# Kernel optimization log

Measured on AMD Instinct MI355X. Metric: run time of the kernel, lower is better.

The kernel has to match this reference:

```python
import jax, jax.numpy as jnp
import numpy as np
from jax import lax

B, C, H, W = 4, 256, 64, 64
O = 256
EPS = 1e-5


def setup_inputs() -> dict:
    key = jax.random.key(0)
    ks = jax.random.split(key, 20)
    s = 0.02
    d = {
        'input1': jax.random.normal(ks[0], (B, C, H, W), jnp.float32),
        'input2': jax.random.normal(ks[1], (B, C, H, W), jnp.float32),
        'wq1': jax.random.normal(ks[2], (C // 8, C), jnp.float32) * s,
        'bq1': jnp.zeros((C // 8,), jnp.float32),
        'wk1': jax.random.normal(ks[3], (C // 4, C), jnp.float32) * s,
        'bk1': jnp.zeros((C // 4,), jnp.float32),
        'wv1': jax.random.normal(ks[4], (C, C), jnp.float32) * s,
        'bv1': jnp.zeros((C,), jnp.float32),
        'wq2': jax.random.normal(ks[5], (C // 8, C), jnp.float32) * s,
        'bq2': jnp.zeros((C // 8,), jnp.float32),
        'wk2': jax.random.normal(ks[6], (C // 4, C), jnp.float32) * s,
        'bk2': jnp.zeros((C // 4,), jnp.float32),
        'wv2': jax.random.normal(ks[7], (C, C), jnp.float32) * s,
        'bv2': jnp.zeros((C,), jnp.float32),
        'gamma': jnp.asarray([0.1], jnp.float32),
        'w_cat': jax.random.normal(ks[8], (O, 2 * C, 3, 3), jnp.float32) * s,
        'bn_scale': jnp.ones((O,), jnp.float32),
        'bn_bias': jnp.zeros((O,), jnp.float32),
        'bn_mean': jnp.zeros((O,), jnp.float32),
        'bn_var': jnp.ones((O,), jnp.float32),
    }
    return d


def _conv1x1(x, w, b):
    # x: [B,C,H,W], w: [Co,C] -> [B,Co,H,W]
    return jnp.einsum('bchw,oc->bohw', x, w) + b[None, :, None, None]


def reference(input1, input2, wq1, bq1, wk1, bk1, wv1, bv1,
              wq2, bq2, wk2, bk2, wv2, bv2, gamma, w_cat,
              bn_scale, bn_bias, bn_mean, bn_var):
    b, c, h, w = input1.shape
    hw = h * w
    q1 = _conv1x1(input1, wq1, bq1)
    k1 = _conv1x1(input1, wk1, bk1).reshape(b, -1, hw)
    v1 = _conv1x1(input1, wv1, bv1).reshape(b, -1, hw)
    q2 = _conv1x1(input2, wq2, bq2)
    k2 = _conv1x1(input2, wk2, bk2).reshape(b, -1, hw)
    v2 = _conv1x1(input2, wv2, bv2).reshape(b, -1, hw)
    # concat q heads along channel -> [B, C/4, HW] -> [B, HW, C/4]
    q = jnp.concatenate([q1, q2], axis=1).reshape(b, -1, hw).transpose(0, 2, 1)
    # branch 1: [B,HW,HW] scores (no scaling, as in source)
    attn1 = jax.nn.softmax(jnp.einsum('bnc,bcm->bnm', q, k1), axis=-1)
    out1 = jnp.einsum('bcm,bnm->bcn', v1, attn1).reshape(b, c, h, w)
    out1 = gamma[0] * out1 + input1
    # branch 2
    attn2 = jax.nn.softmax(jnp.einsum('bnc,bcm->bnm', q, k2), axis=-1)
    out2 = jnp.einsum('bcm,bnm->bcn', v2, attn2).reshape(b, c, h, w)
    out2 = gamma[0] * out2 + input2
    # conv_cat: 3x3 conv (no bias) + BatchNorm (eval stats) + ReLU
    cat = jnp.concatenate([out1, out2], axis=1)
    conv = lax.conv_general_dilated(cat, w_cat, (1, 1), 'SAME',
                                    dimension_numbers=('NCHW', 'OIHW', 'NCHW'))
    inv = bn_scale / jnp.sqrt(bn_var + EPS)
    bn = conv * inv[None, :, None, None] + (bn_bias - bn_mean * inv)[None, :, None, None]
    feat_sum = jax.nn.relu(bn)
    return (feat_sum, out1, out2)
```

## Files before the change

kernel.cpp:

```cpp
#include <hip/hip_runtime.h>
#include <hip/hip_bf16.h>

#define HW 4096

#define KT_OFF   1048576
#define WTP_OFF  1572864
#define O1_OFF   4194304
#define WVB_OFF  1179648

typedef short v8s  __attribute__((ext_vector_type(8)));
typedef float v16f __attribute__((ext_vector_type(16)));

#define LSTR 72
#define ZSTR 264
#define CPAD 20
#define PL_ROWS 128
#define PL_SZ  (2 * PL_ROWS * LSTR)
#define XP_SZ  (2 * 256 * LSTR)

__device__ __forceinline__ unsigned short f2b(float f) {
    unsigned u = __float_as_uint(f);
    return (unsigned short)((u + 0x7fffu + ((u >> 16) & 1u)) >> 16);
}
__device__ __forceinline__ unsigned cvt_pk_bf16(float lo, float hi) {
    float2 f2; f2.x = lo; f2.y = hi;
    __hip_bfloat162 h = __float22bfloat162_rn(f2);
    unsigned r;
    __builtin_memcpy(&r, &h, 4);
    return r;
}
__device__ __forceinline__ v8s load8(const unsigned short* p) {
    union { uint2 u[2]; v8s v; } t;
    t.u[0] = *(const uint2*)p;
    t.u[1] = *(const uint2*)(p + 4);
    return t.v;
}

__global__ __launch_bounds__(256) void wprep_proj(
    const float* __restrict__ wq1, const float* __restrict__ wk1, const float* __restrict__ wv1,
    const float* __restrict__ wq2, const float* __restrict__ wk2, const float* __restrict__ wv2,
    float* __restrict__ wtp) {
    int idx = blockIdx.x * 256 + threadIdx.x;
    if (idx >= 2 * 256 * 352) return;
    int sel = idx / 90112;
    int r   = idx - sel * 90112;
    int c   = r / 352;
    int co  = r - c * 352;
    const float* w; int row;
    if (co < 32)      { w = sel ? wq2 : wq1; row = co; }
    else if (co < 96) { w = sel ? wk2 : wk1; row = co - 32; }
    else              { w = sel ? wv2 : wv1; row = co - 96; }
    wtp[idx] = w[row * 256 + c];
}

__global__ __launch_bounds__(256) void wprep_convw(const float* __restrict__ wcat,
                                                   unsigned short* __restrict__ wt) {
    int i = blockIdx.x * 256 + threadIdx.x;
    if (i >= 32 * 9 * 256 * 16) return;
    const int ci_l = i & 15;
    const int o    = (i >> 4) & 255;
    const int t2   = i >> 12;
    const int tap  = t2 % 9;
    const int chunk = t2 / 9;
    wt[i] = f2b(wcat[((size_t)o * 512 + chunk * 16 + ci_l) * 9 + tap]);
}

__global__ __launch_bounds__(256) void wprep_wv(const float* __restrict__ wv1,
                                                const float* __restrict__ wv2,
                                                unsigned short* __restrict__ out) {
    int i = blockIdx.x * 256 + threadIdx.x;
    if (i >= 131072) return;
    const float* src = (i < 65536) ? wv1 : wv2;
    out[i] = f2b(src[i & 65535]);
}

__global__ __launch_bounds__(256) void proj_kernel(
    const float* __restrict__ x1, const float* __restrict__ x2,
    const float* __restrict__ bq1, const float* __restrict__ bk1,
    const float* __restrict__ bq2, const float* __restrict__ bk2,
    float* __restrict__ dout) {
    __shared__ __align__(16) float xls[256][64];
    const int tile = blockIdx.x, sel = blockIdx.y, b = blockIdx.z;
    const int n0 = tile * 64;
    const float* xb = (sel ? x2 : x1) + (size_t)b * 256 * HW;

    for (int i = threadIdx.x; i < 4096; i += 256) {
        const int row = i >> 4, c4 = (i & 15) * 4;
        *(float4*)&xls[row][c4] = *(const float4*)(xb + (size_t)row * HW + n0 + c4);
    }
    __syncthreads();

    const int n   = threadIdx.x & 63;
    const int cog = __builtin_amdgcn_readfirstlane(threadIdx.x >> 6);
    const float* bq = sel ? bq2 : bq1;
    const float* bk = sel ? bk2 : bk1;
    const float* wc = dout + WTP_OFF + (size_t)sel * 90112;
    unsigned short* qtg = (unsigned short*)dout + (size_t)b * HW * 64;
    unsigned short* ktg = (unsigned short*)dout + KT_OFF + (size_t)(sel * 4 + b) * HW * 64;

    for (int blk = 0; blk < 3; ++blk) {
        const int co0 = cog * 24 + blk * 8;
        float acc[8];
        const float* brow; int r0; bool isq;
        if (co0 < 32) { r0 = co0;      brow = bq; isq = true;  }
        else          { r0 = co0 - 32; brow = bk; isq = false; }
        #pragma unroll
        for (int k = 0; k < 8; ++k) acc[k] = brow[r0 + k];
        #pragma unroll 4
        for (int c = 0; c < 256; ++c) {
            const float xv = xls[c][n];
            const float4 w0 = *(const float4*)(wc + (size_t)c * 352 + co0);
            const float4 w1 = *(const float4*)(wc + (size_t)c * 352 + co0 + 4);
            acc[0] += xv * w0.x; acc[1] += xv * w0.y; acc[2] += xv * w0.z; acc[3] += xv * w0.w;
            acc[4] += xv * w1.x; acc[5] += xv * w1.y; acc[6] += xv * w1.z; acc[7] += xv * w1.w;
        }
        unsigned pk2[4];
        #pragma unroll
        for (int k = 0; k < 4; ++k) pk2[k] = cvt_pk_bf16(acc[2 * k], acc[2 * k + 1]);
        unsigned short* dst = isq ? (qtg + (size_t)(n0 + n) * 64 + sel * 32 + r0)
                                  : (ktg + (size_t)(n0 + n) * 64 + r0);
        *(uint4*)dst = *(const uint4*)pk2;
    }
}

__global__ __launch_bounds__(512, 2) void attn_kernel(
    const float* __restrict__ in1, const float* __restrict__ in2,
    const unsigned short* __restrict__ wvbf,
    const float* __restrict__ bv1, const float* __restrict__ bv2,
    const float* __restrict__ gamma_p,
    float* __restrict__ dout) {
    __shared__ __align__(16) unsigned short smem[PL_SZ + XP_SZ];
    __shared__ float rsums[128][2];
    __shared__ float lfin[128];

    const int qt = blockIdx.x, br = blockIdx.y, b = blockIdx.z;
    const int t = threadIdx.x;
    const int w = t >> 6, lane = t & 63, h = lane >> 5, l32 = lane & 31;

    const unsigned short* qtg = (const unsigned short*)dout + (size_t)b * HW * 64;
    const unsigned short* ktg = (const unsigned short*)dout + KT_OFF + (size_t)(br * 4 + b) * HW * 64;
    const float* xg = (br ? in2 : in1) + (size_t)b * 256 * HW;
    float* zo = dout + O1_OFF + (size_t)br * 4194304 + (size_t)b * 256 * HW;

    const int msub = (w & 1) * 32;
    const int nsub = (w >> 1) * 32;
    const int cs   = w & 3;
    const int nh   = w >> 2;
    const int koff = h * 8;

    unsigned short* plds = smem;
    unsigned short* xp   = smem + PL_SZ;

    v8s aq[4];
    #pragma unroll
    for (int ks = 0; ks < 4; ++ks)
        aq[ks] = *(const v8s*)(qtg + (size_t)(qt * 128 + nsub + l32) * 64 + ks * 16 + koff);

    const unsigned short* kpt = ktg + (size_t)(msub + l32) * 64 + koff;
    v8s kf[4];
    #pragma unroll
    for (int ks = 0; ks < 4; ++ks)
        kf[ks] = *(const v8s*)(kpt + ks * 16);

    const int m4 = (t & 15) * 4, r0i = t >> 4;
    const float* xgp = xg + (size_t)r0i * HW + m4;

    uint2 xpk[8];
    {
        float4 xr0[8];
        #pragma unroll
        for (int j = 0; j < 8; ++j) xr0[j] = *(const float4*)(xgp + (size_t)j * 32 * HW);
        #pragma unroll
        for (int j = 0; j < 8; ++j) {
            xpk[j].x = cvt_pk_bf16(xr0[j].x, xr0[j].y);
            xpk[j].y = cvt_pk_bf16(xr0[j].z, xr0[j].w);
        }
    }

    v16f a00, a01, a10, a11;
    #pragma unroll
    for (int i = 0; i < 16; ++i) { a00[i] = 0.f; a01[i] = 0.f; a10[i] = 0.f; a11[i] = 0.f; }
    float racc = 0.f;

    #pragma unroll 1
    for (int mt = 0; mt < 64; ++mt) {
        const int cur = mt & 1;
        v16f s;
        #pragma unroll
        for (int i = 0; i < 16; ++i) s[i] = 0.f;
        #pragma unroll
        for (int ks = 0; ks < 4; ++ks)
            s = __builtin_amdgcn_mfma_f32_32x32x16_bf16(kf[ks], aq[ks], s, 0, 0, 0);
        const int mg = (mt < 63) ? (mt + 1) * 64 : 0;
        #pragma unroll
        for (int ks = 0; ks < 4; ++ks)
            kf[ks] = *(const v8s*)(kpt + (size_t)mg * 64 + ks * 16);
        float4 xr[8];
        #pragma unroll
        for (int j = 0; j < 8; ++j)
            xr[j] = *(const float4*)(xgp + (size_t)j * 32 * HW + mg);
        unsigned short* prow = plds + (size_t)(cur * PL_ROWS + nsub + l32) * LSTR + msub;
        #pragma unroll
        for (int rp = 0; rp < 8; ++rp) {
            const float e0 = __expf(s[2 * rp]);
            const float e1 = __expf(s[2 * rp + 1]);
            racc += e0 + e1;
            const int m0 = ((2 * rp) & 3) + 8 * (rp >> 1) + 4 * h;
            *(unsigned*)&prow[m0] = cvt_pk_bf16(e0, e1);
        }
        {
            unsigned short* xw = xp + (size_t)(cur * 256 + r0i) * LSTR + m4;
            #pragma unroll
            for (int j = 0; j < 8; ++j)
                *(uint2*)(xw + (size_t)j * 32 * LSTR) = xpk[j];
        }
        __syncthreads();
        {
            const unsigned short* xb0 = xp + (size_t)(cur * 256 + cs * 64 + l32) * LSTR;
            const unsigned short* xb1 = xb0 + (size_t)32 * LSTR;
            const unsigned short* pb0 = plds + (size_t)(cur * PL_ROWS + nh * 64 + l32) * LSTR;
            const unsigned short* pb1 = pb0 + (size_t)32 * LSTR;
            #pragma unroll
            for (int ks = 0; ks < 4; ++ks) {
                const int mo = ks * 16 + koff;
                const v8s xa0 = *(const v8s*)(xb0 + mo);
                const v8s xa1 = *(const v8s*)(xb1 + mo);
                const v8s pf0 = *(const v8s*)(pb0 + mo);
                const v8s pf1 = *(const v8s*)(pb1 + mo);
                a00 = __builtin_amdgcn_mfma_f32_32x32x16_bf16(xa0, pf0, a00, 0, 0, 0);
                a01 = __builtin_amdgcn_mfma_f32_32x32x16_bf16(xa0, pf1, a01, 0, 0, 0);
                a10 = __builtin_amdgcn_mfma_f32_32x32x16_bf16(xa1, pf0, a10, 0, 0, 0);
                a11 = __builtin_amdgcn_mfma_f32_32x32x16_bf16(xa1, pf1, a11, 0, 0, 0);
            }
        }
        #pragma unroll
        for (int j = 0; j < 8; ++j) {
            xpk[j].x = cvt_pk_bf16(xr[j].x, xr[j].y);
            xpk[j].y = cvt_pk_bf16(xr[j].z, xr[j].w);
        }
    }
    __syncthreads();
    {
        const float rtot = racc + __shfl_xor(racc, 32);
        if (lane < 32) rsums[nsub + l32][w & 1] = rtot;
    }
    __syncthreads();
    if (t < 128) lfin[t] = 1.0f / (rsums[t][0] + rsums[t][1]);
    __syncthreads();
    const float dn0 = lfin[nh * 64 + l32];
    const float dn1 = lfin[nh * 64 + 32 + l32];
    unsigned short (*zt)[ZSTR] = (unsigned short (*)[ZSTR])smem;
    #pragma unroll
    for (int rp = 0; rp < 8; ++rp) {
        const int r = rp * 2;
        const int c = cs * 64 + (r & 3) + 8 * (r >> 2) + 4 * h;
        const int n0r = nh * 64 + l32, n1r = nh * 64 + 32 + l32;
        *(unsigned*)&zt[n0r][c]      = cvt_pk_bf16(a00[r] * dn0, a00[r + 1] * dn0);
        *(unsigned*)&zt[n1r][c]      = cvt_pk_bf16(a01[r] * dn1, a01[r + 1] * dn1);
        *(unsigned*)&zt[n0r][c + 32] = cvt_pk_bf16(a10[r] * dn0, a10[r + 1] * dn0);
        *(unsigned*)&zt[n1r][c + 32] = cvt_pk_bf16(a11[r] * dn1, a11[r + 1] * dn1);
    }
    __syncthreads();
    const unsigned short* wvb = wvbf + (size_t)br * 65536;
    const float* bvp = br ? bv2 : bv1;
    const float gamma = gamma_p[0];
    const int ob = cs * 64;
    const int ncol = qt * 128 + nh * 64;
    v16f m00, m01, m10, m11;
    #pragma unroll
    for (int i = 0; i < 16; ++i) { m00[i] = 0.f; m01[i] = 0.f; m10[i] = 0.f; m11[i] = 0.f; }
    #pragma unroll
    for (int ks = 0; ks < 16; ++ks) {
        const int k = ks * 16 + koff;
        const v8s aA = *(const v8s*)(wvb + (size_t)(ob + l32) * 256 + k);
        const v8s aB = *(const v8s*)(wvb + (size_t)(ob + 32 + l32) * 256 + k);
        const v8s b0v = *(const v8s*)&zt[nh * 64 + l32][k];
        const v8s b1v = *(const v8s*)&zt[nh * 64 + 32 + l32][k];
        m00 = __builtin_amdgcn_mfma_f32_32x32x16_bf16(aA, b0v, m00, 0, 0, 0);
        m01 = __builtin_amdgcn_mfma_f32_32x32x16_bf16(aA, b1v, m01, 0, 0, 0);
        m10 = __builtin_amdgcn_mfma_f32_32x32x16_bf16(aB, b0v, m10, 0, 0, 0);
        m11 = __builtin_amdgcn_mfma_f32_32x32x16_bf16(aB, b1v, m11, 0, 0, 0);
    }
    #pragma unroll
    for (int r = 0; r < 16; ++r) {
        const int o = ob + (r & 3) + 8 * (r >> 2) + 4 * h;
        const float bvA = bvp[o], bvB = bvp[o + 32];
        const size_t base0 = (size_t)o * HW + ncol;
        const size_t base1 = (size_t)(o + 32) * HW + ncol;
        zo[base0 + l32]      = gamma * (m00[r] + bvA) + xg[base0 + l32];
        zo[base0 + 32 + l32] = gamma * (m01[r] + bvA) + xg[base0 + 32 + l32];
        zo[base1 + l32]      = gamma * (m10[r] + bvB) + xg[base1 + l32];
        zo[base1 + 32 + l32] = gamma * (m11[r] + bvB) + xg[base1 + 32 + l32];
    }
}

__global__ __launch_bounds__(256) void conv_kernel(
    const unsigned short* __restrict__ wt,
    const float* __restrict__ bn_scale, const float* __restrict__ bn_bias,
    const float* __restrict__ bn_mean,  const float* __restrict__ bn_var,
    float* __restrict__ dout) {
    __shared__ __align__(16) unsigned short xl[4][66][CPAD];
    __shared__ __align__(16) unsigned short wl[9][64][CPAD];

    const int pt = blockIdx.x;
    const int ot = blockIdx.y;
    const int b  = blockIdx.z;
    const int h0 = pt * 2;
    const int t  = threadIdx.x;
    const int w  = t >> 6, lane = t & 63, h = lane >> 5, l32 = lane & 31;
    const int osub = (w & 1) * 32;
    const int ps0  = (w >> 1) * 64;

    int ldsoff[9], srcoff[9]; bool valid[9], inb[9];
    #pragma unroll
    for (int k = 0; k < 9; ++k) {
        const int i = t + k * 256;
        valid[k] = i < 2112;
        const int col = i % 66, rem = i / 66;
        const int row = rem & 3, cp = rem >> 2;
        const int hh = h0 + row - 1, ww = col - 1;
        inb[k] = (hh >= 0 && hh < 64 && ww >= 0 && ww < 64);
        srcoff[k] = 2 * cp * HW + (inb[k] ? hh * 64 + ww : 0);
        ldsoff[k] = (row * 66 + col) * CPAD + 2 * cp;
    }
    unsigned short* xlf = &xl[0][0][0];

    float inv[16], add[16];
    #pragma unroll
    for (int r = 0; r < 16; ++r) {
        const int o_g = ot * 64 + osub + (r & 3) + 8 * (r >> 2) + 4 * h;
        const float iv = bn_scale[o_g] * __frsqrt_rn(bn_var[o_g] + 1e-5f);
        inv[r] = iv;
        add[r] = bn_bias[o_g] - bn_mean[o_g] * iv;
    }

    v16f acc0, acc1;
    #pragma unroll
    for (int i = 0; i < 16; ++i) { acc0[i] = 0.f; acc1[i] = 0.f; }

    #pragma unroll 1
    for (int chunk = 0; chunk < 32; ++chunk) {
        const float* src = dout + O1_OFF + (size_t)(chunk < 16 ? 0 : 1) * 4194304
                         + (size_t)b * 1048576 + (size_t)((chunk & 15) * 16) * HW;
        const unsigned short* wsl = wt + (size_t)chunk * 36864 + (size_t)(ot * 64) * 16;
        __syncthreads();
        #pragma unroll
        for (int k = 0; k < 9; ++k) {
            if (valid[k]) {
                float v0 = 0.f, v1 = 0.f;
                if (inb[k]) {
                    const float* p = src + srcoff[k];
                    v0 = p[0]; v1 = p[HW];
                }
                *(unsigned*)&xlf[ldsoff[k]] = cvt_pk_bf16(v0, v1);
            }
        }
        #pragma unroll
        for (int u9 = 0; u9 < 9; ++u9) {
            const int u = t + u9 * 256;
            const int tap = u >> 8, rem2 = u & 255;
            const int o = rem2 >> 2, q = rem2 & 3;
            const uint2 wv = *(const uint2*)(wsl + ((size_t)tap * 256 + o) * 16 + q * 4);
            *(uint2*)&wl[tap][o][q * 4] = wv;
        }
        __syncthreads();
        #pragma unroll
        for (int dy = 0; dy < 3; ++dy) {
            #pragma unroll
            for (int dx = 0; dx < 3; ++dx) {
                const v8s af = load8(&wl[dy * 3 + dx][osub + l32][h * 8]);
                const int n0 = ps0 + l32, n1 = ps0 + 32 + l32;
                const v8s b0 = load8(&xl[(n0 >> 6) + dy][(n0 & 63) + dx][h * 8]);
                const v8s b1 = load8(&xl[(n1 >> 6) + dy][(n1 & 63) + dx][h * 8]);
                acc0 = __builtin_amdgcn_mfma_f32_32x32x16_bf16(af, b0, acc0, 0, 0, 0);
                acc1 = __builtin_amdgcn_mfma_f32_32x32x16_bf16(af, b1, acc1, 0, 0, 0);
            }
        }
    }
    const int px0 = ps0 + l32, px1 = ps0 + 32 + l32;
    const size_t gpx0 = (size_t)(h0 + (px0 >> 6)) * 64 + (px0 & 63);
    const size_t gpx1 = (size_t)(h0 + (px1 >> 6)) * 64 + (px1 & 63);
    #pragma unroll
    for (int r = 0; r < 16; ++r) {
        const int o_g = ot * 64 + osub + (r & 3) + 8 * (r >> 2) + 4 * h;
        const size_t obase = ((size_t)b * 256 + o_g) * HW;
        float v0 = acc0[r] * inv[r] + add[r];
        float v1 = acc1[r] * inv[r] + add[r];
        v0 = v0 > 0.f ? v0 : 0.f;
        v1 = v1 > 0.f ? v1 : 0.f;
        dout[obase + gpx0] = v0;
        dout[obase + gpx1] = v1;
    }
}

extern "C" void kernel_launch(void* const* d_in, const int* in_sizes, int n_in,
                              void* d_out, int out_size, void* d_ws, size_t ws_size,
                              hipStream_t stream) {
    (void)in_sizes; (void)n_in; (void)out_size; (void)ws_size;
    const float* x1   = (const float*)d_in[0];
    const float* x2   = (const float*)d_in[1];
    const float* wq1  = (const float*)d_in[2];
    const float* bq1  = (const float*)d_in[3];
    const float* wk1  = (const float*)d_in[4];
    const float* bk1  = (const float*)d_in[5];
    const float* wv1  = (const float*)d_in[6];
    const float* bv1  = (const float*)d_in[7];
    const float* wq2  = (const float*)d_in[8];
    const float* bq2  = (const float*)d_in[9];
    const float* wk2  = (const float*)d_in[10];
    const float* bk2  = (const float*)d_in[11];
    const float* wv2  = (const float*)d_in[12];
    const float* bv2  = (const float*)d_in[13];
    const float* gma  = (const float*)d_in[14];
    const float* wcat = (const float*)d_in[15];
    const float* bns  = (const float*)d_in[16];
    const float* bnb  = (const float*)d_in[17];
    const float* bnm  = (const float*)d_in[18];
    const float* bnv  = (const float*)d_in[19];

    float* out = (float*)d_out;
    unsigned short* wtc = (unsigned short*)d_ws;
    unsigned short* wvb = wtc + WVB_OFF;

    wprep_proj<<<704, 256, 0, stream>>>(wq1, wk1, wv1, wq2, wk2, wv2, out + WTP_OFF);
    wprep_convw<<<4608, 256, 0, stream>>>(wcat, wtc);
    wprep_wv<<<512, 256, 0, stream>>>(wv1, wv2, wvb);
    proj_kernel<<<dim3(64, 2, 4), 256, 0, stream>>>(x1, x2, bq1, bk1, bq2, bk2, out);
    attn_kernel<<<dim3(32, 2, 4), 512, 0, stream>>>(x1, x2, wvb, bv1, bv2, gma, out);
    conv_kernel<<<dim3(32, 4, 4), 256, 0, stream>>>(wtc, bns, bnb, bnm, bnv, out);
}
```

Baseline: 475.6 us.

## Double-buffer conv LDS tiles and prefetch next chunk into registers

The 3x3 conv kernel now keeps two LDS buffers for the input and weight tiles. Each chunk's global loads are issued into registers before the MFMA loop of the previous chunk, so memory latency can overlap compute, and one of the two barriers per chunk is removed. In exchange it doubles LDS use and adds about 27 live registers, which may lower occupancy.

Result: faster. 411.4 us (-13.5%).

```diff
diff --git a/kernel.cpp b/kernel.cpp
--- a/kernel.cpp
+++ b/kernel.cpp
@@ -17,6 +17,7 @@
 #define PL_ROWS 128
 #define PL_SZ  (2 * PL_ROWS * LSTR)
 #define XP_SZ  (2 * 256 * LSTR)
+#define XLHALF (4 * 66 * CPAD)
 
 __device__ __forceinline__ unsigned short f2b(float f) {
     unsigned u = __float_as_uint(f);
@@ -299,8 +300,8 @@
     const float* __restrict__ bn_scale, const float* __restrict__ bn_bias,
     const float* __restrict__ bn_mean,  const float* __restrict__ bn_var,
     float* __restrict__ dout) {
-    __shared__ __align__(16) unsigned short xl[4][66][CPAD];
-    __shared__ __align__(16) unsigned short wl[9][64][CPAD];
+    __shared__ __align__(16) unsigned short xl[2][4][66][CPAD];
+    __shared__ __align__(16) unsigned short wl[2][9][64][CPAD];
 
     const int pt = blockIdx.x;
     const int ot = blockIdx.y;
@@ -323,7 +324,7 @@
         srcoff[k] = 2 * cp * HW + (inb[k] ? hh * 64 + ww : 0);
         ldsoff[k] = (row * 66 + col) * CPAD + 2 * cp;
     }
-    unsigned short* xlf = &xl[0][0][0];
+    unsigned short* xlf = &xl[0][0][0][0];
 
     float inv[16], add[16];
     #pragma unroll
@@ -338,21 +339,19 @@
     #pragma unroll
     for (int i = 0; i < 16; ++i) { acc0[i] = 0.f; acc1[i] = 0.f; }
 
-    #pragma unroll 1
-    for (int chunk = 0; chunk < 32; ++chunk) {
-        const float* src = dout + O1_OFF + (size_t)(chunk < 16 ? 0 : 1) * 4194304
-                         + (size_t)b * 1048576 + (size_t)((chunk & 15) * 16) * HW;
-        const unsigned short* wsl = wt + (size_t)chunk * 36864 + (size_t)(ot * 64) * 16;
-        __syncthreads();
+    const float* bsrc = dout + O1_OFF + (size_t)b * 1048576;
+    const unsigned short* wbase = wt + (size_t)(ot * 64) * 16;
+
+    float xv0[9], xv1[9];
+    uint2 wr[9];
+    {
+        const float* src = bsrc;
         #pragma unroll
         for (int k = 0; k < 9; ++k) {
-            if (valid[k]) {
-                float v0 = 0.f, v1 = 0.f;
-                if (inb[k]) {
-                    const float* p = src + srcoff[k];
-                    v0 = p[0]; v1 = p[HW];
-                }
-                *(unsigned*)&xlf[ldsoff[k]] = cvt_pk_bf16(v0, v1);
+            xv0[k] = 0.f; xv1[k] = 0.f;
+            if (valid[k] && inb[k]) {
+                const float* p = src + srcoff[k];
+                xv0[k] = p[0]; xv1[k] = p[HW];
             }
         }
         #pragma unroll
@@ -360,18 +359,54 @@
             const int u = t + u9 * 256;
             const int tap = u >> 8, rem2 = u & 255;
             const int o = rem2 >> 2, q = rem2 & 3;
-            const uint2 wv = *(const uint2*)(wsl + ((size_t)tap * 256 + o) * 16 + q * 4);
-            *(uint2*)&wl[tap][o][q * 4] = wv;
+            wr[u9] = *(const uint2*)(wbase + ((size_t)tap * 256 + o) * 16 + q * 4);
+        }
+    }
+
+    #pragma unroll 1
+    for (int chunk = 0; chunk < 32; ++chunk) {
+        const int cur = chunk & 1;
+        #pragma unroll
+        for (int k = 0; k < 9; ++k)
+            if (valid[k])
+                *(unsigned*)&xlf[cur * XLHALF + ldsoff[k]] = cvt_pk_bf16(xv0[k], xv1[k]);
+        #pragma unroll
+        for (int u9 = 0; u9 < 9; ++u9) {
+            const int u = t + u9 * 256;
+            const int tap = u >> 8, rem2 = u & 255;
+            const int o = rem2 >> 2, q = rem2 & 3;
+            *(uint2*)&wl[cur][tap][o][q * 4] = wr[u9];
+        }
+        if (chunk < 31) {
+            const int cn = chunk + 1;
+            const float* src = bsrc + (size_t)(cn < 16 ? 0 : 1) * 4194304
+                             + (size_t)((cn & 15) * 16) * HW;
+            #pragma unroll
+            for (int k = 0; k < 9; ++k) {
+                xv0[k] = 0.f; xv1[k] = 0.f;
+                if (valid[k] && inb[k]) {
+                    const float* p = src + srcoff[k];
+                    xv0[k] = p[0]; xv1[k] = p[HW];
+                }
+            }
+            const unsigned short* wsl = wbase + (size_t)cn * 36864;
+            #pragma unroll
+            for (int u9 = 0; u9 < 9; ++u9) {
+                const int u = t + u9 * 256;
+                const int tap = u >> 8, rem2 = u & 255;
+                const int o = rem2 >> 2, q = rem2 & 3;
+                wr[u9] = *(const uint2*)(wsl + ((size_t)tap * 256 + o) * 16 + q * 4);
+            }
         }
         __syncthreads();
         #pragma unroll
         for (int dy = 0; dy < 3; ++dy) {
             #pragma unroll
             for (int dx = 0; dx < 3; ++dx) {
-                const v8s af = load8(&wl[dy * 3 + dx][osub + l32][h * 8]);
+                const v8s af = load8(&wl[cur][dy * 3 + dx][osub + l32][h * 8]);
                 const int n0 = ps0 + l32, n1 = ps0 + 32 + l32;
-                const v8s b0 = load8(&xl[(n0 >> 6) + dy][(n0 & 63) + dx][h * 8]);
-                const v8s b1 = load8(&xl[(n1 >> 6) + dy][(n1 & 63) + dx][h * 8]);
+                const v8s b0 = load8(&xl[cur][(n0 >> 6) + dy][(n0 & 63) + dx][h * 8]);
+                const v8s b1 = load8(&xl[cur][(n1 >> 6) + dy][(n1 & 63) + dx][h * 8]);
                 acc0 = __builtin_amdgcn_mfma_f32_32x32x16_bf16(af, b0, acc0, 0, 0, 0);
                 acc1 = __builtin_amdgcn_mfma_f32_32x32x16_bf16(af, b1, acc1, 0, 0, 0);
             }
```

## Restructure conv kernel with register weights, double-buffered LDS prefetch, and XCD-aware block mapping

Applied to the files above, without the earlier changes.

The conv kernel now tiles one output row per block, which quadruples the grid to 1024 blocks. Weight fragments are loaded straight from global memory into registers instead of being staged through LDS. The input tile is double-buffered in LDS, and the next chunk is prefetched into registers so only one barrier is needed per chunk. Both attn and conv blocks are remapped through a linear block index to group work across XCDs for L2 locality. The cost is more redundant global weight reads per block, since each block holds only one accumulator, and higher register pressure under the new launch bounds.

Result: faster. 414.8 us (-12.8%).

```diff
diff --git a/kernel.cpp b/kernel.cpp
--- a/kernel.cpp
+++ b/kernel.cpp
@@ -13,10 +13,12 @@
 
 #define LSTR 72
 #define ZSTR 264
-#define CPAD 20
 #define PL_ROWS 128
 #define PL_SZ  (2 * PL_ROWS * LSTR)
 #define XP_SZ  (2 * 256 * LSTR)
+#define CPAD2 24
+#define XSLOT 198
+#define XLH2  (XSLOT * CPAD2)
 
 __device__ __forceinline__ unsigned short f2b(float f) {
     unsigned u = __float_as_uint(f);
@@ -133,7 +135,10 @@
     __shared__ float rsums[128][2];
     __shared__ float lfin[128];
 
-    const int qt = blockIdx.x, br = blockIdx.y, b = blockIdx.z;
+    const int bid = blockIdx.x;
+    const int g   = bid & 7;
+    const int qt  = bid >> 3;
+    const int br  = g >> 2, b = g & 3;
     const int t = threadIdx.x;
     const int w = t >> 6, lane = t & 63, h = lane >> 5, l32 = lane & 31;
 
@@ -294,102 +299,101 @@
     }
 }
 
-__global__ __launch_bounds__(256) void conv_kernel(
+__global__ __launch_bounds__(256, 4) void conv_kernel(
     const unsigned short* __restrict__ wt,
     const float* __restrict__ bn_scale, const float* __restrict__ bn_bias,
     const float* __restrict__ bn_mean,  const float* __restrict__ bn_var,
     float* __restrict__ dout) {
-    __shared__ __align__(16) unsigned short xl[4][66][CPAD];
-    __shared__ __align__(16) unsigned short wl[9][64][CPAD];
-
-    const int pt = blockIdx.x;
-    const int ot = blockIdx.y;
-    const int b  = blockIdx.z;
-    const int h0 = pt * 2;
-    const int t  = threadIdx.x;
-    const int w  = t >> 6, lane = t & 63, h = lane >> 5, l32 = lane & 31;
+    __shared__ __align__(16) unsigned short xl[2][XLH2];
+
+    const int bid = blockIdx.x;
+    const int lin = (bid & 7) * 128 + (bid >> 3);
+    const int ot  = lin & 3;
+    const int rowb = lin >> 2;
+    const int h0  = rowb & 63;
+    const int b   = rowb >> 6;
+    const int t   = threadIdx.x;
+    const int w   = t >> 6, lane = t & 63, h = lane >> 5, l32 = lane & 31;
     const int osub = (w & 1) * 32;
-    const int ps0  = (w >> 1) * 64;
-
-    int ldsoff[9], srcoff[9]; bool valid[9], inb[9];
-    #pragma unroll
-    for (int k = 0; k < 9; ++k) {
-        const int i = t + k * 256;
-        valid[k] = i < 2112;
-        const int col = i % 66, rem = i / 66;
-        const int row = rem & 3, cp = rem >> 2;
+    const int px0  = (w >> 1) * 32;
+
+    int ldsoff[7], srcoff[7]; bool act[7], inb[7];
+    #pragma unroll
+    for (int k = 0; k < 7; ++k) {
+        const int u = t + k * 256;
+        act[k] = u < 1584;
+        const int pix = u % 198, grp = u / 198;
+        const int row = pix / 66, col = pix % 66;
         const int hh = h0 + row - 1, ww = col - 1;
-        inb[k] = (hh >= 0 && hh < 64 && ww >= 0 && ww < 64);
-        srcoff[k] = 2 * cp * HW + (inb[k] ? hh * 64 + ww : 0);
-        ldsoff[k] = (row * 66 + col) * CPAD + 2 * cp;
-    }
-    unsigned short* xlf = &xl[0][0][0];
-
-    float inv[16], add[16];
+        inb[k] = act[k] && (hh >= 0 && hh < 64 && ww >= 0 && ww < 64);
+        srcoff[k] = 2 * grp * HW + (inb[k] ? hh * 64 + ww : 0);
+        ldsoff[k] = pix * CPAD2 + 2 * grp;
+    }
+
+    v16f acc;
+    #pragma unroll
+    for (int i = 0; i < 16; ++i) acc[i] = 0.f;
+
+    const float* bsrc = dout + O1_OFF + (size_t)b * 1048576;
+    const unsigned short* wbase = wt + (size_t)(ot * 64 + osub + l32) * 16 + h * 8;
+
+    float xv0[7], xv1[7];
+    #pragma unroll
+    for (int k = 0; k < 7; ++k) {
+        xv0[k] = 0.f; xv1[k] = 0.f;
+        if (inb[k]) {
+            const float* p = bsrc + srcoff[k];
+            xv0[k] = p[0]; xv1[k] = p[HW];
+        }
+    }
+
+    #pragma unroll 1
+    for (int chunk = 0; chunk < 32; ++chunk) {
+        const int cur = chunk & 1;
+        v8s wf[9];
+        {
+            const unsigned short* wc = wbase + (size_t)chunk * 36864;
+            #pragma unroll
+            for (int tap = 0; tap < 9; ++tap)
+                wf[tap] = *(const v8s*)(wc + (size_t)tap * 4096);
+        }
+        #pragma unroll
+        for (int k = 0; k < 7; ++k)
+            if (act[k])
+                *(unsigned*)&xl[cur][ldsoff[k]] = cvt_pk_bf16(xv0[k], xv1[k]);
+        if (chunk < 31) {
+            const int cn = chunk + 1;
+            const float* src = bsrc + (size_t)(cn < 16 ? 0 : 1) * 4194304
+                             + (size_t)((cn & 15) * 16) * HW;
+            #pragma unroll
+            for (int k = 0; k < 7; ++k) {
+                xv0[k] = 0.f; xv1[k] = 0.f;
+                if (inb[k]) {
+                    const float* p = src + srcoff[k];
+                    xv0[k] = p[0]; xv1[k] = p[HW];
+                }
+            }
+        }
+        __syncthreads();
+        #pragma unroll
+        for (int dy = 0; dy < 3; ++dy) {
+            #pragma unroll
+            for (int dx = 0; dx < 3; ++dx) {
+                const v8s bf = *(const v8s*)&xl[cur][(dy * 66 + px0 + l32 + dx) * CPAD2 + h * 8];
+                acc = __builtin_amdgcn_mfma_f32_32x32x16_bf16(wf[dy * 3 + dx], bf, acc, 0, 0, 0);
+            }
+        }
+    }
+    const int px = px0 + l32;
+    const size_t gp = (size_t)h0 * 64 + px;
     #pragma unroll
     for (int r = 0; r < 16; ++r) {
         const int o_g = ot * 64 + osub + (r & 3) + 8 * (r >> 2) + 4 * h;
         const float iv = bn_scale[o_g] * __frsqrt_rn(bn_var[o_g] + 1e-5f);
-        inv[r] = iv;
-        add[r] = bn_bias[o_g] - bn_mean[o_g] * iv;
-    }
-
-    v16f acc0, acc1;
-    #pragma unroll
-    for (int i = 0; i < 16; ++i) { acc0[i] = 0.f; acc1[i] = 0.f; }
-
-    #pragma unroll 1
-    for (int chunk = 0; chunk < 32; ++chunk) {
-        const float* src = dout + O1_OFF + (size_t)(chunk < 16 ? 0 : 1) * 4194304
-                         + (size_t)b * 1048576 + (size_t)((chunk & 15) * 16) * HW;
-        const unsigned short* wsl = wt + (size_t)chunk * 36864 + (size_t)(ot * 64) * 16;
-        __syncthreads();
-        #pragma unroll
-        for (int k = 0; k < 9; ++k) {
-            if (valid[k]) {
-                float v0 = 0.f, v1 = 0.f;
-                if (inb[k]) {
-                    const float* p = src + srcoff[k];
-                    v0 = p[0]; v1 = p[HW];
-                }
-                *(unsigned*)&xlf[ldsoff[k]] = cvt_pk_bf16(v0, v1);
-            }
-        }
-        #pragma unroll
-        for (int u9 = 0; u9 < 9; ++u9) {
-            const int u = t + u9 * 256;
-            const int tap = u >> 8, rem2 = u & 255;
-            const int o = rem2 >> 2, q = rem2 & 3;
-            const uint2 wv = *(const uint2*)(wsl + ((size_t)tap * 256 + o) * 16 + q * 4);
-            *(uint2*)&wl[tap][o][q * 4] = wv;
-        }
-        __syncthreads();
-        #pragma unroll
-        for (int dy = 0; dy < 3; ++dy) {
-            #pragma unroll
-            for (int dx = 0; dx < 3; ++dx) {
-                const v8s af = load8(&wl[dy * 3 + dx][osub + l32][h * 8]);
-                const int n0 = ps0 + l32, n1 = ps0 + 32 + l32;
-                const v8s b0 = load8(&xl[(n0 >> 6) + dy][(n0 & 63) + dx][h * 8]);
-                const v8s b1 = load8(&xl[(n1 >> 6) + dy][(n1 & 63) + dx][h * 8]);
-                acc0 = __builtin_amdgcn_mfma_f32_32x32x16_bf16(af, b0, acc0, 0, 0, 0);
-                acc1 = __builtin_amdgcn_mfma_f32_32x32x16_bf16(af, b1, acc1, 0, 0, 0);
-            }
-        }
-    }
-    const int px0 = ps0 + l32, px1 = ps0 + 32 + l32;
-    const size_t gpx0 = (size_t)(h0 + (px0 >> 6)) * 64 + (px0 & 63);
-    const size_t gpx1 = (size_t)(h0 + (px1 >> 6)) * 64 + (px1 & 63);
-    #pragma unroll
-    for (int r = 0; r < 16; ++r) {
-        const int o_g = ot * 64 + osub + (r & 3) + 8 * (r >> 2) + 4 * h;
-        const size_t obase = ((size_t)b * 256 + o_g) * HW;
-        float v0 = acc0[r] * inv[r] + add[r];
-        float v1 = acc1[r] * inv[r] + add[r];
-        v0 = v0 > 0.f ? v0 : 0.f;
-        v1 = v1 > 0.f ? v1 : 0.f;
-        dout[obase + gpx0] = v0;
-        dout[obase + gpx1] = v1;
+        const float ad = bn_bias[o_g] - bn_mean[o_g] * iv;
+        float v = acc[r] * iv + ad;
+        v = v > 0.f ? v : 0.f;
+        dout[((size_t)b * 256 + o_g) * HW + gp] = v;
     }
 }
 
@@ -426,6 +430,6 @@
     wprep_convw<<<4608, 256, 0, stream>>>(wcat, wtc);
     wprep_wv<<<512, 256, 0, stream>>>(wv1, wv2, wvb);
     proj_kernel<<<dim3(64, 2, 4), 256, 0, stream>>>(x1, x2, bq1, bk1, bq2, bk2, out);
-    attn_kernel<<<dim3(32, 2, 4), 512, 0, stream>>>(x1, x2, wvb, bv1, bv2, gma, out);
-    conv_kernel<<<dim3(32, 4, 4), 256, 0, stream>>>(wtc, bns, bnb, bnm, bnv, out);
-}
+    attn_kernel<<<256, 512, 0, stream>>>(x1, x2, wvb, bv1, bv2, gma, out);
+    conv_kernel<<<1024, 256, 0, stream>>>(wtc, bns, bnb, bnm, bnv, out);
+}
```
